# Kernel optimization log

Hardware: AMD Instinct MI355X
Metric: run time of the kernel (lower is better)

Reference implementation:

```python
import jax, jax.numpy as jnp
import numpy as np

N_QUBITS = 12
DIM = 2 ** N_QUBITS  # 4096

_H = (jnp.array([[1.0, 1.0], [1.0, -1.0]]) / np.sqrt(2.0)).astype(jnp.complex64)
_X = jnp.array([[0.0, 1.0], [1.0, 0.0]], dtype=jnp.complex64)


def setup_inputs() -> dict:
    key = jax.random.key(0)
    k1, k2 = jax.random.split(key)
    state = jax.random.normal(k1, (8, 512, DIM), dtype=jnp.float32)
    params = jax.random.normal(k2, (N_QUBITS,), dtype=jnp.float32)
    return {"state": state, "params": params}


def _to_quantum(x):
    # faithful to _classical_to_quantum_inspired: normalize, phase = acos(|v|), sign * exp(i*phase)
    norms = jnp.linalg.norm(x, axis=-1, keepdims=True)
    v = x / (norms + 1e-8)
    mag = jnp.minimum(jnp.abs(v), 1.0)
    q = (jnp.sign(v) * jnp.exp(1j * jnp.arccos(mag))).astype(jnp.complex64)
    nrm = jnp.sqrt(jnp.sum(q.real ** 2 + q.imag ** 2, axis=-1, keepdims=True))
    return q / nrm.astype(jnp.complex64)


def _axis(q):
    # qubit q = bit q (LSB); tensor axes ordered MSB-first after batch axis 0
    return 1 + (N_QUBITS - 1 - q)


def _apply_1q(full, q, U):
    ax = _axis(q)
    moved = jnp.moveaxis(full, ax, -1)
    out = jnp.einsum('...b,ab->...a', moved, U)
    return jnp.moveaxis(out, -1, ax)


def _apply_ctrl(full, c, t, U):
    # apply U on target qubit t where control qubit c == 1
    axc = _axis(c)
    b0 = jnp.take(full, 0, axis=axc)
    b1 = jnp.take(full, 1, axis=axc)
    axt = _axis(t)
    axt_sub = axt - 1 if axt > axc else axt
    moved = jnp.moveaxis(b1, axt_sub, -1)
    b1n = jnp.moveaxis(jnp.einsum('...b,ab->...a', moved, U), -1, axt_sub)
    return jnp.stack([b0, b1n], axis=axc)


def _rx(theta):
    c = jnp.cos(theta / 2).astype(jnp.complex64)
    s = (-1j * jnp.sin(theta / 2)).astype(jnp.complex64)
    return jnp.stack([jnp.stack([c, s]), jnp.stack([s, c])])


def reference(state, params):
    B, T, D = state.shape
    psi = _to_quantum(state.reshape(B * T, D))  # (N, 2**n) complex64
    full = psi.reshape((B * T,) + (2,) * N_QUBITS)
    for q in range(N_QUBITS):
        full = _apply_1q(full, q, _H)                                  # Hadamard
        full = _apply_ctrl(full, q, (q + 1) % N_QUBITS, _rx(params[q]))  # controlled-RX
        if q < N_QUBITS - 1:
            full = _apply_ctrl(full, q, q + 1, _X)                     # CNOT
    amp = full.reshape(B * T, D)
    probs = amp.real ** 2 + amp.imag ** 2  # measurement probabilities
    return probs.reshape(B, T, D).astype(jnp.float32)
```

## Files before the change

### kernel.cpp

```cpp
#include <hip/hip_runtime.h>

#define NQ  12
#define DIM 4096
#define TPB 256

__device__ __forceinline__ int SW(int i) { return i ^ ((i >> 5) & 31); }

__device__ __forceinline__ float wave_reduce(float v) {
#pragma unroll
    for (int m = 32; m >= 1; m >>= 1) v += __shfl_xor(v, m, 64);
    return v;
}

#define BCAST(v, q) __uint_as_float(__builtin_amdgcn_readlane(__float_as_uint(v), (q)))

template <int MC, int MT, bool XGATE>
__device__ __forceinline__ void apply_layer(float2* a, float ct, float sn) {
#pragma unroll
    for (int i = 0; i < 16; ++i) {
        if (i & MC) continue;
        const int j = i | MC;
        const float2 t0 = a[i], t1 = a[j];
        a[i] = make_float2(t0.x + t1.x, t0.y + t1.y);
        a[j] = make_float2(t0.x - t1.x, t0.y - t1.y);
    }
#pragma unroll
    for (int i = 0; i < 16; ++i) {
        if (!(i & MC) || (i & MT)) continue;
        const int j = i | MT;
        const float2 b0 = a[i], b1 = a[j];
        const float s0x = sn * b0.y, s0y = -sn * b0.x;
        const float s1x = sn * b1.y, s1y = -sn * b1.x;
        if (XGATE) {
            a[i] = make_float2(fmaf(ct, b1.x, s0x), fmaf(ct, b1.y, s0y));
            a[j] = make_float2(fmaf(ct, b0.x, s1x), fmaf(ct, b0.y, s1y));
        } else {
            a[i] = make_float2(fmaf(ct, b0.x, s1x), fmaf(ct, b0.y, s1y));
            a[j] = make_float2(fmaf(ct, b1.x, s0x), fmaf(ct, b1.y, s0y));
        }
    }
}

__global__ __launch_bounds__(TPB) void qlayer_kernel(
        const float* __restrict__ state, const float* __restrict__ params,
        float* __restrict__ out) {
    __shared__ float sre[DIM];
    __shared__ float sim[DIM];

    const int t = threadIdx.x;
    const int lane = t & 63;
    const long long sbase = (long long)blockIdx.x * DIM;

    const float th = params[lane < NQ ? lane : 0] * 0.5f;
    const float cl = cosf(th);
    const float sl = sinf(th);

    float x[16];
    const float4* gp = (const float4*)(state + sbase + t * 16);
    float ss = 0.f;
#pragma unroll
    for (int j = 0; j < 4; ++j) {
        const float4 v = gp[j];
        x[4 * j + 0] = v.x; x[4 * j + 1] = v.y;
        x[4 * j + 2] = v.z; x[4 * j + 3] = v.w;
        ss = fmaf(v.x, v.x, ss); ss = fmaf(v.y, v.y, ss);
        ss = fmaf(v.z, v.z, ss); ss = fmaf(v.w, v.w, ss);
    }
    ss = wave_reduce(ss);
    if (lane == 0) sre[t >> 6] = ss;
    __syncthreads();
    const float nrm  = sqrtf(sre[0] + sre[1] + sre[2] + sre[3]);
    const float invd = 1.0f / (nrm + 1e-8f);
    __syncthreads();

    float2 a[16];
#pragma unroll
    for (int k = 0; k < 16; ++k) {
        const float v   = x[k] * invd;
        const float re  = fminf(fmaxf(v, -1.0f), 1.0f);
        const float imb = sqrtf(fmaxf(1.0f - re * re, 0.f));
        const float im  = (v > 0.f) ? imb : ((v < 0.f) ? -imb : 0.f);
        a[k] = make_float2(re, im);
    }

    apply_layer<1, 2, true>(a, BCAST(cl, 0), BCAST(sl, 0));
    apply_layer<2, 4, true>(a, BCAST(cl, 1), BCAST(sl, 1));
    apply_layer<4, 8, true>(a, BCAST(cl, 2), BCAST(sl, 2));
#pragma unroll
    for (int r = 0; r < 16; ++r) {
        const int s = SW(t * 16 + r);
        sre[s] = a[r].x; sim[s] = a[r].y;
    }
    __syncthreads();

    {
        const int base = (t & 7) | ((t >> 3) << 7);
#pragma unroll
        for (int r = 0; r < 16; ++r) {
            const int s = SW(base | (r << 3));
            a[r] = make_float2(sre[s], sim[s]);
        }
        apply_layer<1, 2, true>(a, BCAST(cl, 3), BCAST(sl, 3));
        apply_layer<2, 4, true>(a, BCAST(cl, 4), BCAST(sl, 4));
        apply_layer<4, 8, true>(a, BCAST(cl, 5), BCAST(sl, 5));
#pragma unroll
        for (int r = 0; r < 16; ++r) {
            const int s = SW(base | (r << 3));
            sre[s] = a[r].x; sim[s] = a[r].y;
        }
    }
    __syncthreads();

    {
        const int base = (t & 63) | ((t >> 6) << 10);
#pragma unroll
        for (int r = 0; r < 16; ++r) {
            const int s = SW(base | (r << 6));
            a[r] = make_float2(sre[s], sim[s]);
        }
        apply_layer<1, 2, true>(a, BCAST(cl, 6), BCAST(sl, 6));
        apply_layer<2, 4, true>(a, BCAST(cl, 7), BCAST(sl, 7));
        apply_layer<4, 8, true>(a, BCAST(cl, 8), BCAST(sl, 8));
#pragma unroll
        for (int r = 0; r < 16; ++r) {
            const int s = SW(base | (r << 6));
            sre[s] = a[r].x; sim[s] = a[r].y;
        }
    }
    __syncthreads();

    {
        const int base = t << 1;
#pragma unroll
        for (int r = 0; r < 16; ++r) {
            const int s = SW(base | ((r & 7) << 9) | (r >> 3));
            a[r] = make_float2(sre[s], sim[s]);
        }
        apply_layer<1, 2, true >(a, BCAST(cl, 9),  BCAST(sl, 9));
        apply_layer<2, 4, true >(a, BCAST(cl, 10), BCAST(sl, 10));
        apply_layer<4, 8, false>(a, BCAST(cl, 11), BCAST(sl, 11));

        const float scale = 0x1p-24f;
        float2* outp = (float2*)(out + sbase);
#pragma unroll
        for (int r = 0; r < 8; ++r) {
            const int idx = base | ((r & 7) << 9);
            const float p0 = (a[r].x * a[r].x + a[r].y * a[r].y) * scale;
            const float p1 = (a[r | 8].x * a[r | 8].x + a[r | 8].y * a[r | 8].y) * scale;
            outp[idx >> 1] = make_float2(p0, p1);
        }
    }
}

extern "C" void kernel_launch(void* const* d_in, const int* in_sizes, int n_in,
                              void* d_out, int out_size, void* d_ws, size_t ws_size,
                              hipStream_t stream) {
    (void)in_sizes; (void)n_in; (void)out_size; (void)d_ws; (void)ws_size;
    const float* state  = (const float*)d_in[0];
    const float* params = (const float*)d_in[1];
    float* out = (float*)d_out;
    qlayer_kernel<<<dim3(4096), dim3(TPB), 0, stream>>>(state, params, out);
}
```

Baseline: 128.7 us.

## Use packed float2 vector math and per-stage LDS swizzles

Rewrites the gate butterflies on ext_vector_type(2) floats so the compiler can emit packed FP32 instructions (v_pk_add/v_pk_fma) for the complex adds and multiply-adds. It also changes the LDS XOR swizzle per stage, using a shift of 4 or 5 depending on the access stride, to reduce bank conflicts, and reuses the swizzled addresses between the load and the store in stage two. The swizzle read and write pairs must match for correctness. Packed ops may add swizzle moves for the .yx operand.

```diff
diff --git a/kernel.cpp b/kernel.cpp
--- a/kernel.cpp
+++ b/kernel.cpp
@@ -4,7 +4,10 @@
 #define DIM 4096
 #define TPB 256
 
-__device__ __forceinline__ int SW(int i) { return i ^ ((i >> 5) & 31); }
+typedef float v2f __attribute__((ext_vector_type(2)));
+
+__device__ __forceinline__ int SW4(int i) { return i ^ ((i >> 4) & 31); }
+__device__ __forceinline__ int SW5(int i) { return i ^ ((i >> 5) & 31); }
 
 __device__ __forceinline__ float wave_reduce(float v) {
 #pragma unroll
@@ -15,28 +18,28 @@
 #define BCAST(v, q) __uint_as_float(__builtin_amdgcn_readlane(__float_as_uint(v), (q)))
 
 template <int MC, int MT, bool XGATE>
-__device__ __forceinline__ void apply_layer(float2* a, float ct, float sn) {
+__device__ __forceinline__ void apply_layer(v2f* a, v2f ctv, v2f snv) {
 #pragma unroll
     for (int i = 0; i < 16; ++i) {
         if (i & MC) continue;
         const int j = i | MC;
-        const float2 t0 = a[i], t1 = a[j];
-        a[i] = make_float2(t0.x + t1.x, t0.y + t1.y);
-        a[j] = make_float2(t0.x - t1.x, t0.y - t1.y);
+        const v2f t0 = a[i], t1 = a[j];
+        a[i] = t0 + t1;
+        a[j] = t0 - t1;
     }
 #pragma unroll
     for (int i = 0; i < 16; ++i) {
         if (!(i & MC) || (i & MT)) continue;
         const int j = i | MT;
-        const float2 b0 = a[i], b1 = a[j];
-        const float s0x = sn * b0.y, s0y = -sn * b0.x;
-        const float s1x = sn * b1.y, s1y = -sn * b1.x;
+        const v2f b0 = a[i], b1 = a[j];
+        const v2f s0 = snv * b0.yx;
+        const v2f s1 = snv * b1.yx;
         if (XGATE) {
-            a[i] = make_float2(fmaf(ct, b1.x, s0x), fmaf(ct, b1.y, s0y));
-            a[j] = make_float2(fmaf(ct, b0.x, s1x), fmaf(ct, b0.y, s1y));
+            a[i] = ctv * b1 + s0;
+            a[j] = ctv * b0 + s1;
         } else {
-            a[i] = make_float2(fmaf(ct, b0.x, s1x), fmaf(ct, b0.y, s1y));
-            a[j] = make_float2(fmaf(ct, b1.x, s0x), fmaf(ct, b1.y, s0y));
+            a[i] = ctv * b0 + s1;
+            a[j] = ctv * b1 + s0;
         }
     }
 }
@@ -73,40 +76,45 @@
     const float invd = 1.0f / (nrm + 1e-8f);
     __syncthreads();
 
-    float2 a[16];
+    v2f a[16];
 #pragma unroll
     for (int k = 0; k < 16; ++k) {
         const float v   = x[k] * invd;
         const float re  = fminf(fmaxf(v, -1.0f), 1.0f);
         const float imb = sqrtf(fmaxf(1.0f - re * re, 0.f));
         const float im  = (v > 0.f) ? imb : ((v < 0.f) ? -imb : 0.f);
-        a[k] = make_float2(re, im);
+        v2f q; q.x = re; q.y = im;
+        a[k] = q;
     }
 
-    apply_layer<1, 2, true>(a, BCAST(cl, 0), BCAST(sl, 0));
-    apply_layer<2, 4, true>(a, BCAST(cl, 1), BCAST(sl, 1));
-    apply_layer<4, 8, true>(a, BCAST(cl, 2), BCAST(sl, 2));
+#define CTV(q) ({ v2f _c; _c.x = BCAST(cl, q); _c.y = _c.x; _c; })
+#define SNV(q) ({ float _s = BCAST(sl, q); v2f _v; _v.x = _s; _v.y = -_s; _v; })
+
+    apply_layer<1, 2, true>(a, CTV(0), SNV(0));
+    apply_layer<2, 4, true>(a, CTV(1), SNV(1));
+    apply_layer<4, 8, true>(a, CTV(2), SNV(2));
 #pragma unroll
     for (int r = 0; r < 16; ++r) {
-        const int s = SW(t * 16 + r);
+        const int s = SW4(t * 16 + r);
         sre[s] = a[r].x; sim[s] = a[r].y;
     }
     __syncthreads();
 
     {
         const int base = (t & 7) | ((t >> 3) << 7);
+        int sa[16];
 #pragma unroll
         for (int r = 0; r < 16; ++r) {
-            const int s = SW(base | (r << 3));
-            a[r] = make_float2(sre[s], sim[s]);
+            sa[r] = SW4(base | (r << 3));
+            v2f q; q.x = sre[sa[r]]; q.y = sim[sa[r]];
+            a[r] = q;
         }
-        apply_layer<1, 2, true>(a, BCAST(cl, 3), BCAST(sl, 3));
-        apply_layer<2, 4, true>(a, BCAST(cl, 4), BCAST(sl, 4));
-        apply_layer<4, 8, true>(a, BCAST(cl, 5), BCAST(sl, 5));
+        apply_layer<1, 2, true>(a, CTV(3), SNV(3));
+        apply_layer<2, 4, true>(a, CTV(4), SNV(4));
+        apply_layer<4, 8, true>(a, CTV(5), SNV(5));
 #pragma unroll
         for (int r = 0; r < 16; ++r) {
-            const int s = SW(base | (r << 3));
-            sre[s] = a[r].x; sim[s] = a[r].y;
+            sre[sa[r]] = a[r].x; sim[sa[r]] = a[r].y;
         }
     }
     __syncthreads();
@@ -115,15 +123,16 @@
         const int base = (t & 63) | ((t >> 6) << 10);
 #pragma unroll
         for (int r = 0; r < 16; ++r) {
-            const int s = SW(base | (r << 6));
-            a[r] = make_float2(sre[s], sim[s]);
+            const int s = SW4(base | (r << 6));
+            v2f q; q.x = sre[s]; q.y = sim[s];
+            a[r] = q;
         }
-        apply_layer<1, 2, true>(a, BCAST(cl, 6), BCAST(sl, 6));
-        apply_layer<2, 4, true>(a, BCAST(cl, 7), BCAST(sl, 7));
-        apply_layer<4, 8, true>(a, BCAST(cl, 8), BCAST(sl, 8));
+        apply_layer<1, 2, true>(a, CTV(6), SNV(6));
+        apply_layer<2, 4, true>(a, CTV(7), SNV(7));
+        apply_layer<4, 8, true>(a, CTV(8), SNV(8));
 #pragma unroll
         for (int r = 0; r < 16; ++r) {
-            const int s = SW(base | (r << 6));
+            const int s = SW5(base | (r << 6));
             sre[s] = a[r].x; sim[s] = a[r].y;
         }
     }
@@ -133,23 +142,27 @@
         const int base = t << 1;
 #pragma unroll
         for (int r = 0; r < 16; ++r) {
-            const int s = SW(base | ((r & 7) << 9) | (r >> 3));
-            a[r] = make_float2(sre[s], sim[s]);
+            const int s = SW5(base | ((r & 7) << 9) | (r >> 3));
+            v2f q; q.x = sre[s]; q.y = sim[s];
+            a[r] = q;
         }
-        apply_layer<1, 2, true >(a, BCAST(cl, 9),  BCAST(sl, 9));
-        apply_layer<2, 4, true >(a, BCAST(cl, 10), BCAST(sl, 10));
-        apply_layer<4, 8, false>(a, BCAST(cl, 11), BCAST(sl, 11));
+        apply_layer<1, 2, true >(a, CTV(9),  SNV(9));
+        apply_layer<2, 4, true >(a, CTV(10), SNV(10));
+        apply_layer<4, 8, false>(a, CTV(11), SNV(11));
 
         const float scale = 0x1p-24f;
         float2* outp = (float2*)(out + sbase);
 #pragma unroll
         for (int r = 0; r < 8; ++r) {
             const int idx = base | ((r & 7) << 9);
-            const float p0 = (a[r].x * a[r].x + a[r].y * a[r].y) * scale;
-            const float p1 = (a[r | 8].x * a[r | 8].x + a[r | 8].y * a[r | 8].y) * scale;
-            outp[idx >> 1] = make_float2(p0, p1);
+            const v2f q0 = a[r] * a[r];
+            const v2f q1 = a[r | 8] * a[r | 8];
+            outp[idx >> 1] = make_float2((q0.x + q0.y) * scale,
+                                         (q1.x + q1.y) * scale);
         }
     }
+#undef CTV
+#undef SNV
 }
 
 extern "C" void kernel_launch(void* const* d_in, const int* in_sizes, int n_in,
```

After: 126.9 us. About the same (-1.4%).
